# Optimization experiments

Measured on AMD Instinct MI355X. Metric: run time of the kernel, lower is better.

The kernel has to match this reference:

```python
import jax, jax.numpy as jnp
import numpy as np

B, T, C = 8, 2048, 512
H = 8
DH = C // H
MLP = 4 * C
EPS = 1e-5


def _ln(x, w, b):
    m = jnp.mean(x, axis=-1, keepdims=True)
    v = jnp.mean(jnp.square(x - m), axis=-1, keepdims=True)
    return (x - m) * jax.lax.rsqrt(v + EPS) * w + b


def setup_inputs() -> dict:
    key = jax.random.key(0)
    ks = jax.random.split(key, 12)
    s = 0.02
    return {
        "x": jax.random.normal(ks[0], (B, T, C), jnp.float32),
        "c": jax.random.normal(ks[1], (B, C), jnp.float32),
        "qkv_w": jax.random.normal(ks[2], (3 * C, C), jnp.float32) * s,
        "qkv_b": jnp.zeros((3 * C,), jnp.float32),
        "proj_w": jax.random.normal(ks[3], (C, C), jnp.float32) * s,
        "proj_b": jnp.zeros((C,), jnp.float32),
        "ada_w": jax.random.normal(ks[4], (6 * C, C), jnp.float32) * s,
        "ada_b": jnp.zeros((6 * C,), jnp.float32),
        "fc1_w": jax.random.normal(ks[5], (MLP, C), jnp.float32) * s,
        "fc1_b": jnp.zeros((MLP,), jnp.float32),
        "fc2_w": jax.random.normal(ks[6], (C, MLP), jnp.float32) * s,
        "fc2_b": jnp.zeros((C,), jnp.float32),
        "ln1_w": jnp.ones((C,), jnp.float32),
        "ln1_b": jnp.zeros((C,), jnp.float32),
        "ln2_w": jnp.ones((C,), jnp.float32),
        "ln2_b": jnp.zeros((C,), jnp.float32),
    }


def reference(x, c, qkv_w, qkv_b, proj_w, proj_b, ada_w, ada_b,
              fc1_w, fc1_b, fc2_w, fc2_b, ln1_w, ln1_b, ln2_w, ln2_b):
    # AdaLN modulation: SiLU -> Linear -> chunk into 6 [B,C] pieces
    mod = jax.nn.silu(c) @ ada_w.T + ada_b  # [B, 6C]
    sh_msa, sc_msa, g_msa, sh_mlp, sc_mlp, g_mlp = jnp.split(mod, 6, axis=1)

    # --- attention branch ---
    h = _ln(x, ln1_w, ln1_b) * (1.0 + sc_msa[:, None, :]) + sh_msa[:, None, :]
    qkv = h @ qkv_w.T + qkv_b  # [B, T, 3C]
    q, k, v = jnp.split(qkv, 3, axis=-1)
    q = q.reshape(B, T, H, DH).transpose(0, 2, 1, 3)  # [B,H,T,Dh]
    k = k.reshape(B, T, H, DH).transpose(0, 2, 1, 3)
    v = v.reshape(B, T, H, DH).transpose(0, 2, 1, 3)
    scores = jnp.einsum('bhqd,bhkd->bhqk', q, k) * (1.0 / np.sqrt(DH))
    w = jax.nn.softmax(scores, axis=-1)
    o = jnp.einsum('bhqk,bhkd->bhqd', w, v)  # [B,H,T,Dh]
    o = o.transpose(0, 2, 1, 3).reshape(B, T, C)
    attn = o @ proj_w.T + proj_b
    x = x + g_msa[:, None, :] * attn

    # --- MLP branch ---
    h2 = _ln(x, ln2_w, ln2_b) * (1.0 + sc_mlp[:, None, :]) + sh_mlp[:, None, :]
    m = jax.nn.gelu(h2 @ fc1_w.T + fc1_b, approximate=True) @ fc2_w.T + fc2_b
    return x + g_mlp[:, None, :] * m
```

## Files before the change

kernel.cpp:

```cpp
#include <hip/hip_runtime.h>
#include <cstdint>
#include <cstddef>

typedef unsigned short u16;
typedef short v8s __attribute__((ext_vector_type(8)));
typedef float v4f __attribute__((ext_vector_type(4)));
typedef float f32x16 __attribute__((ext_vector_type(16)));
typedef unsigned int v4u __attribute__((ext_vector_type(4)));
typedef unsigned int v2u __attribute__((ext_vector_type(2)));
typedef unsigned short v4u16 __attribute__((ext_vector_type(4)));

#define TT 2048
#define CC 512

#define QSCALE 0.18033688011112042f

__device__ __forceinline__ u16 f2bf(float f) {
    unsigned u = __float_as_uint(f);
    u += 0x7fffu + ((u >> 16) & 1u);
    return (u16)(u >> 16);
}

__device__ __forceinline__ unsigned cvt_pk_bf16(float lo, float hi) {
    unsigned r;
    asm("v_cvt_pk_bf16_f32 %0, %1, %2" : "=v"(r) : "v"(lo), "v"(hi));
    return r;
}

__device__ __forceinline__ void swap32(unsigned a, unsigned b, unsigned& x, unsigned& y) {
#if __has_builtin(__builtin_amdgcn_permlane32_swap)
    auto r = __builtin_amdgcn_permlane32_swap(a, b, false, false);
    x = r[0]; y = r[1];
#else
    unsigned bx = (unsigned)__shfl_xor((int)b, 32, 64);
    unsigned ax = (unsigned)__shfl_xor((int)a, 32, 64);
    bool hi5 = (threadIdx.x & 32) != 0;
    x = hi5 ? bx : a;
    y = hi5 ? b : ax;
#endif
}

__device__ __forceinline__ void gl2lds16(const void* g, void* l) {
    __builtin_amdgcn_global_load_lds(
        (const __attribute__((address_space(1))) unsigned int*)g,
        (__attribute__((address_space(3))) unsigned int*)l,
        16, 0, 0);
}

__global__ __launch_bounds__(256) void f2bf_k(const float* __restrict__ s,
                                              u16* __restrict__ d, int n) {
    int i = (blockIdx.x * 256 + threadIdx.x) * 4;
    if (i >= n) return;
    float4 v = *(const float4*)(s + i);
    v4u16 r;
    r[0] = f2bf(v.x); r[1] = f2bf(v.y); r[2] = f2bf(v.z); r[3] = f2bf(v.w);
    *(v4u16*)(d + i) = r;
}

__global__ __launch_bounds__(256) void ada_kernel(const float* __restrict__ c,
                                                  const float* __restrict__ W,
                                                  const float* __restrict__ bias,
                                                  float* __restrict__ mod) {
    int idx = blockIdx.x * 4 + (threadIdx.x >> 6);
    int l = threadIdx.x & 63;
    int bb = idx / 3072;
    int n = idx - bb * 3072;
    const float* cp = c + bb * CC;
    const float* wp = W + (size_t)n * CC;
    float s = 0.f;
    #pragma unroll
    for (int i = 0; i < 8; ++i) {
        int k = l * 8 + i;
        float cv = cp[k];
        float sil = cv / (1.f + __expf(-cv));
        s += sil * wp[k];
    }
    #pragma unroll
    for (int off = 32; off; off >>= 1) s += __shfl_xor(s, off, 64);
    if (l == 0) mod[idx] = s + bias[n];
}

__global__ __launch_bounds__(256) void ln_mod_kernel(const float* __restrict__ X,
                                                     const float* __restrict__ lnw,
                                                     const float* __restrict__ lnb,
                                                     const float* __restrict__ mod,
                                                     int sh_off, int sc_off,
                                                     u16* __restrict__ out) {
    int row = blockIdx.x * 4 + (threadIdx.x >> 6);
    int l = threadIdx.x & 63;
    int b = row >> 11;
    const float* xr = X + (size_t)row * CC + l * 8;
    float4 va = *(const float4*)(xr);
    float4 vb = *(const float4*)(xr + 4);
    float v[8] = {va.x, va.y, va.z, va.w, vb.x, vb.y, vb.z, vb.w};
    float s = 0.f;
    #pragma unroll
    for (int i = 0; i < 8; ++i) s += v[i];
    #pragma unroll
    for (int off = 32; off; off >>= 1) s += __shfl_xor(s, off, 64);
    float mean = s * (1.f / CC);
    float q = 0.f;
    #pragma unroll
    for (int i = 0; i < 8; ++i) { float d = v[i] - mean; q += d * d; }
    #pragma unroll
    for (int off = 32; off; off >>= 1) q += __shfl_xor(q, off, 64);
    float rstd = rsqrtf(q * (1.f / CC) + 1e-5f);
    int col = l * 8;
    const float* shp = mod + b * 3072 + sh_off + col;
    const float* scp = mod + b * 3072 + sc_off + col;
    v8s st;
    #pragma unroll
    for (int i = 0; i < 8; ++i) {
        float hv = (v[i] - mean) * rstd * lnw[col + i] + lnb[col + i];
        float r = hv * (1.f + scp[i]) + shp[i];
        st[i] = (short)f2bf(r);
    }
    *(v8s*)(out + (size_t)row * CC + col) = st;
}

template <int MODE>
__global__ __launch_bounds__(256)
void gemm_bt(const u16* __restrict__ A, const u16* __restrict__ W,
             const float* __restrict__ bias, void* __restrict__ outp,
             const float* __restrict__ resid, const float* __restrict__ gate,
             int NX, int N, int K) {
    __shared__ alignas(16) u16 Al[2][4096];
    __shared__ alignas(16) u16 Bl[2][4096];
    const int id = blockIdx.x;
    const int wg = (id & 7) * (gridDim.x >> 3) + (id >> 3);
    const int by = wg / NX, bx = wg - by * NX;
    const int bn = bx << 7, bm = by << 7;
    const int tid = threadIdx.x;
    const int w = tid >> 6, l = tid & 63;
    const int hi = l >> 4, lo = l & 15;
    const int wr = (w >> 1) << 6, wc = (w & 1) << 6;

    v4f acc[4][4] = {};

    const int srow = l >> 2;
    const int sp = l & 3;
    const int NT = K >> 5;

    auto stage = [&](int buf, int kt) {
        const int k0 = kt << 5;
        #pragma unroll
        for (int i = 0; i < 2; ++i) {
            const int c = w + (i << 2);
            const int row = (c << 4) + srow;
            const int lg = sp ^ ((row >> 1) & 3);
            gl2lds16(A + (size_t)(bm + row) * K + k0 + (lg << 3), &Al[buf][c << 9]);
            gl2lds16(W + (size_t)(bn + row) * K + k0 + (lg << 3), &Bl[buf][c << 9]);
        }
    };

    stage(0, 0);
    __syncthreads();
    int cur = 0;
    for (int t = 0; t < NT; ++t) {
        if (t + 1 < NT) stage(cur ^ 1, t + 1);
        const u16* Ab = Al[cur];
        const u16* Bb = Bl[cur];
        v8s aF[4], bF[4];
        #pragma unroll
        for (int mi = 0; mi < 4; ++mi) {
            int r = wr + (mi << 4) + lo;
            aF[mi] = *(const v8s*)(Ab + (r << 5) + ((hi ^ ((r >> 1) & 3)) << 3));
        }
        #pragma unroll
        for (int ni = 0; ni < 4; ++ni) {
            int r = wc + (ni << 4) + lo;
            bF[ni] = *(const v8s*)(Bb + (r << 5) + ((hi ^ ((r >> 1) & 3)) << 3));
        }
        #pragma unroll
        for (int mi = 0; mi < 4; ++mi)
            #pragma unroll
            for (int ni = 0; ni < 4; ++ni)
                acc[mi][ni] = __builtin_amdgcn_mfma_f32_16x16x32_bf16(
                    aF[mi], bF[ni], acc[mi][ni], 0, 0, 0);
        __syncthreads();
        cur ^= 1;
    }

    #pragma unroll
    for (int mi = 0; mi < 4; ++mi) {
        #pragma unroll
        for (int ni = 0; ni < 4; ++ni) {
            int col = bn + wc + (ni << 4) + lo;
            float bv = bias[col];
            #pragma unroll
            for (int j = 0; j < 4; ++j) {
                int row = bm + wr + (mi << 4) + hi * 4 + j;
                float v = acc[mi][ni][j] + bv;
                if constexpr (MODE == 0) {
                    float sc2 = (col < 512) ? QSCALE : 1.0f;
                    ((u16*)outp)[(size_t)row * N + col] = f2bf(v * sc2);
                } else if constexpr (MODE == 1) {
                    float u2 = 1.5957691216057308f * (v + 0.044715f * v * v * v);
                    float g = v / (1.f + __expf(-u2));
                    ((u16*)outp)[(size_t)row * N + col] = f2bf(g);
                } else {
                    float r = resid[(size_t)row * N + col];
                    float gt = gate[(row >> 11) * 3072 + col];
                    ((float*)outp)[(size_t)row * N + col] = r + gt * v;
                }
            }
        }
    }
}

__global__ __launch_bounds__(512, 4)
void attn_kernel(const u16* __restrict__ qkv, u16* __restrict__ O) {
    __shared__ alignas(16) u16 smem[18432];
    const int tid = threadIdx.x;
    const int w = tid >> 6, l = tid & 63;
    const int l31 = l & 31, l5 = l >> 5;
    const int id = blockIdx.x;
    const int bh = id & 63, b = bh >> 3, h = bh & 7;
    const int qt = id >> 6;

    const int qrow = qt * 256 + w * 32 + l31;
    const u16* qp = qkv + (size_t)(b * TT + qrow) * 1536 + h * 64;
    v8s qf[4];
    #pragma unroll
    for (int ks = 0; ks < 4; ++ks) qf[ks] = *(const v8s*)(qp + ks * 16 + l5 * 8);

    const int krow8 = l >> 3;
    const int kc = (l & 7) ^ krow8 ^ w;
    const u16* kptr = qkv + (size_t)(b * TT + 8 * w + krow8) * 1536 + 512 + h * 64 + kc * 8;

    const int grp = tid >> 5, d2 = tid & 31;
    const u16* vptr = qkv + (size_t)(b * TT + 4 * grp) * 1536 + 1024 + h * 64 + 2 * d2;

    unsigned V2[4];
    auto loadV = [&](const u16* vp2) {
        #pragma unroll
        for (int e = 0; e < 4; ++e)
            V2[e] = *(const unsigned*)(vp2 + (size_t)e * 1536);
    };
    auto writeV = [&](int buf) {
        char* Vb = (char*)(smem + 8192 + buf * 4096);
        #pragma unroll
        for (int p = 0; p < 2; ++p) {
            int d = 2 * d2 + p;
            int phys = (grp >> 1) ^ (d & 7) ^ ((d >> 3) & 7);
            v2u wv;
            wv[0] = p ? ((V2[0] >> 16) | (V2[1] & 0xffff0000u))
                      : ((V2[0] & 0xffffu) | (V2[1] << 16));
            wv[1] = p ? ((V2[2] >> 16) | (V2[3] & 0xffff0000u))
                      : ((V2[2] & 0xffffu) | (V2[3] << 16));
            *(v2u*)(Vb + d * 128 + phys * 16 + (grp & 1) * 8) = wv;
        }
    };

    auto afrag = [&](const char* base, int t, int ks) -> v8s {
        int row = t * 32 + l31;
        int phys = ((ks << 1) + l5) ^ (row & 7) ^ ((row >> 3) & 7);
        return *(const v8s*)(base + row * 128 + phys * 16);
    };

    v8s onesf;
    #pragma unroll
    for (int i = 0; i < 8; ++i) onesf[i] = (short)0x3F80;

    gl2lds16(kptr, smem + w * 512);
    loadV(vptr);
    writeV(0);
    __syncthreads();

    f32x16 o[2] = {};
    f32x16 lacc = {};

    #pragma unroll 2
    for (int kt = 0; kt < 32; ++kt) {
        const int cur = kt & 1;
        if (kt + 1 < 32) {
            gl2lds16(kptr + (size_t)(kt + 1) * 64 * 1536, smem + (cur ^ 1) * 4096 + w * 512);
            loadV(vptr + (size_t)(kt + 1) * 64 * 1536);
        }
        const char* Kb = (const char*)(smem + cur * 4096);
        const char* Vb = (const char*)(smem + 8192 + cur * 4096);

        f32x16 st[2];
        st[0] = (f32x16)0.f; st[1] = (f32x16)0.f;
        __builtin_amdgcn_s_setprio(1);
        #pragma unroll
        for (int ks = 0; ks < 4; ++ks) {
            v8s k0 = afrag(Kb, 0, ks);
            v8s k1 = afrag(Kb, 1, ks);
            st[0] = __builtin_amdgcn_mfma_f32_32x32x16_bf16(k0, qf[ks], st[0], 0, 0, 0);
            st[1] = __builtin_amdgcn_mfma_f32_32x32x16_bf16(k1, qf[ks], st[1], 0, 0, 0);
        }
        __builtin_amdgcn_s_setprio(0);

        #pragma unroll
        for (int t2 = 0; t2 < 2; ++t2)
            #pragma unroll
            for (int r = 0; r < 16; ++r)
                st[t2][r] = __builtin_exp2f(st[t2][r]);

        __builtin_amdgcn_s_setprio(1);
        #pragma unroll
        for (int ks = 0; ks < 4; ++ks) {
            const int tt = ks >> 1, rb = (ks & 1) * 8;
            unsigned pkA = cvt_pk_bf16(st[tt][rb + 0], st[tt][rb + 1]);
            unsigned pkB = cvt_pk_bf16(st[tt][rb + 4], st[tt][rb + 5]);
            unsigned pkC = cvt_pk_bf16(st[tt][rb + 2], st[tt][rb + 3]);
            unsigned pkD = cvt_pk_bf16(st[tt][rb + 6], st[tt][rb + 7]);
            unsigned w0, w1, w2, w3;
            swap32(pkA, pkB, w0, w2);
            swap32(pkC, pkD, w1, w3);
            v4u pw; pw[0] = w0; pw[1] = w1; pw[2] = w2; pw[3] = w3;
            v8s pa = __builtin_bit_cast(v8s, pw);
            v8s vf0 = afrag(Vb, 0, ks);
            v8s vf1 = afrag(Vb, 1, ks);
            o[0] = __builtin_amdgcn_mfma_f32_32x32x16_bf16(vf0, pa, o[0], 0, 0, 0);
            o[1] = __builtin_amdgcn_mfma_f32_32x32x16_bf16(vf1, pa, o[1], 0, 0, 0);
            lacc = __builtin_amdgcn_mfma_f32_32x32x16_bf16(onesf, pa, lacc, 0, 0, 0);
        }
        __builtin_amdgcn_s_setprio(0);

        if (kt + 1 < 32) writeV(cur ^ 1);
        __syncthreads();
    }

    float inv = 1.f / lacc[0];
    char* outw = (char*)smem + w * 4608;
    #pragma unroll
    for (int t2 = 0; t2 < 2; ++t2)
        #pragma unroll
        for (int r = 0; r < 16; r += 2) {
            int dh = t2 * 32 + (r & 3) + ((r >> 2) << 3) + (l5 << 2);
            unsigned pk = cvt_pk_bf16(o[t2][r] * inv, o[t2][r + 1] * inv);
            *(unsigned*)(outw + l31 * 144 + dh * 2) = pk;
        }
    __syncthreads();
    #pragma unroll
    for (int i = 0; i < 4; ++i) {
        int idx = (i << 9) + tid;
        int qq = idx >> 3, cch = idx & 7;
        v8s vd = *(const v8s*)((char*)smem + (qq >> 5) * 4608 + (qq & 31) * 144 + cch * 16);
        *(v8s*)(O + (size_t)(b * TT + qt * 256 + qq) * 512 + h * 64 + cch * 8) = vd;
    }
}

extern "C" void kernel_launch(void* const* d_in, const int* in_sizes, int n_in,
                              void* d_out, int out_size, void* d_ws, size_t ws_size,
                              hipStream_t stream) {
    const float* x = (const float*)d_in[0];
    const float* c = (const float*)d_in[1];
    const float* qkv_w = (const float*)d_in[2];
    const float* qkv_b = (const float*)d_in[3];
    const float* proj_w = (const float*)d_in[4];
    const float* proj_b = (const float*)d_in[5];
    const float* ada_w = (const float*)d_in[6];
    const float* ada_b = (const float*)d_in[7];
    const float* fc1_w = (const float*)d_in[8];
    const float* fc1_b = (const float*)d_in[9];
    const float* fc2_w = (const float*)d_in[10];
    const float* fc2_b = (const float*)d_in[11];
    const float* ln1_w = (const float*)d_in[12];
    const float* ln1_b = (const float*)d_in[13];
    const float* ln2_w = (const float*)d_in[14];
    const float* ln2_b = (const float*)d_in[15];

    char* p = (char*)d_ws;
    auto carve = [&](size_t bytes) -> char* {
        char* r = p;
        p += (bytes + 255) & ~(size_t)255;
        return r;
    };
    float* mod  = (float*)carve((size_t)8 * 3072 * 4);
    u16* hbuf   = (u16*)carve((size_t)16384 * 512 * 2);
    u16* qkvb   = (u16*)carve((size_t)16384 * 1536 * 2);
    u16* attno  = (u16*)carve((size_t)16384 * 512 * 2);
    float* x1   = (float*)carve((size_t)16384 * 512 * 4);
    u16* wq     = (u16*)carve((size_t)1536 * 512 * 2);
    u16* wpj    = (u16*)carve((size_t)512 * 512 * 2);
    u16* w1     = (u16*)carve((size_t)2048 * 512 * 2);
    u16* w2     = (u16*)carve((size_t)512 * 2048 * 2);
    u16* fc1g   = qkvb;

    f2bf_k<<<(1536 * 512) / 1024, 256, 0, stream>>>(qkv_w, wq, 1536 * 512);
    f2bf_k<<<(512 * 512) / 1024, 256, 0, stream>>>(proj_w, wpj, 512 * 512);
    f2bf_k<<<(2048 * 512) / 1024, 256, 0, stream>>>(fc1_w, w1, 2048 * 512);
    f2bf_k<<<(512 * 2048) / 1024, 256, 0, stream>>>(fc2_w, w2, 512 * 2048);

    ada_kernel<<<24576 / 4, 256, 0, stream>>>(c, ada_w, ada_b, mod);

    ln_mod_kernel<<<16384 / 4, 256, 0, stream>>>(x, ln1_w, ln1_b, mod, 0, 512, hbuf);
    gemm_bt<0><<<12 * 128, 256, 0, stream>>>(hbuf, wq, qkv_b, qkvb,
                                             nullptr, nullptr, 12, 1536, 512);
    attn_kernel<<<512, 512, 0, stream>>>(qkvb, attno);
    gemm_bt<2><<<4 * 128, 256, 0, stream>>>(attno, wpj, proj_b, x1,
                                            x, mod + 2 * 512, 4, 512, 512);

    ln_mod_kernel<<<16384 / 4, 256, 0, stream>>>(x1, ln2_w, ln2_b, mod, 3 * 512, 4 * 512, hbuf);
    gemm_bt<1><<<16 * 128, 256, 0, stream>>>(hbuf, w1, fc1_b, fc1g,
                                             nullptr, nullptr, 16, 2048, 512);
    gemm_bt<2><<<4 * 128, 256, 0, stream>>>(fc1g, w2, fc2_b, (float*)d_out,
                                            x1, mod + 5 * 512, 4, 512, 2048);
}
```

Before: 317.1 us.

## Split attention over key halves, pre-transpose V, use polynomial exp2

Attention now splits the key range into two halves, doubling the grid to 1024 blocks. Each block writes unnormalized partial outputs and row sums, and a new combine kernel adds and normalizes them. A separate kernel pre-transposes V so both K and V can be staged straight into LDS with async global-to-LDS loads, replacing the register shuffle of V. The hardware exp2 is replaced by a cubic polynomial approximation. The changes add two extra launches and extra memory traffic, and lower the accuracy of exp and of the bf16 partial outputs. Scratch buffers (x1, hbuf, wq) are reused for the partials, which is safe only because of launch ordering. Reusing wq for lpart looks wrong, though: wq still holds the QKV weights, which are not needed after the QKV GEMM, so it is fine.

Result: slower. 333.7 us (+5.2%).

```diff
diff --git a/kernel.cpp b/kernel.cpp
--- a/kernel.cpp
+++ b/kernel.cpp
@@ -7,7 +7,6 @@
 typedef float v4f __attribute__((ext_vector_type(4)));
 typedef float f32x16 __attribute__((ext_vector_type(16)));
 typedef unsigned int v4u __attribute__((ext_vector_type(4)));
-typedef unsigned int v2u __attribute__((ext_vector_type(2)));
 typedef unsigned short v4u16 __attribute__((ext_vector_type(4)));
 
 #define TT 2048
@@ -21,10 +20,25 @@
     return (u16)(u >> 16);
 }
 
+__device__ __forceinline__ float bf2f(u16 v) {
+    return __uint_as_float(((unsigned)v) << 16);
+}
+
 __device__ __forceinline__ unsigned cvt_pk_bf16(float lo, float hi) {
     unsigned r;
     asm("v_cvt_pk_bf16_f32 %0, %1, %2" : "=v"(r) : "v"(lo), "v"(hi));
     return r;
+}
+
+__device__ __forceinline__ float fexp2(float x) {
+    float xf = __builtin_floorf(x);
+    float f = x - xf;
+    float p = __builtin_fmaf(f,
+              __builtin_fmaf(f,
+              __builtin_fmaf(f, 0.0781455737f, 0.2261731467f),
+                                0.6955568569f), 1.0f);
+    int e = (int)xf;
+    return __uint_as_float(__float_as_uint(p) + ((unsigned)(e << 23)));
 }
 
 __device__ __forceinline__ void swap32(unsigned a, unsigned b, unsigned& x, unsigned& y) {
@@ -116,6 +130,24 @@
         st[i] = (short)f2bf(r);
     }
     *(v8s*)(out + (size_t)row * CC + col) = st;
+}
+
+__global__ __launch_bounds__(512) void vt_kernel(const u16* __restrict__ qkv,
+                                                 u16* __restrict__ vT) {
+    __shared__ u16 tile[64 * 72];
+    const int id = blockIdx.x;
+    const int bh = id >> 5, tt = id & 31;
+    const int b = bh >> 3, h = bh & 7;
+    const int tid = threadIdx.x;
+    const int tr = tid >> 3, d0 = (tid & 7) * 8;
+    v8s v = *(const v8s*)(qkv + (size_t)(b * TT + tt * 64 + tr) * 1536 + 1024 + h * 64 + d0);
+    *(v8s*)(&tile[tr * 72 + d0]) = v;
+    __syncthreads();
+    const int dr = tid >> 3, t0 = (tid & 7) * 8;
+    v8s ov;
+    #pragma unroll
+    for (int e = 0; e < 8; ++e) ov[e] = (short)tile[(t0 + e) * 72 + dr];
+    *(v8s*)(vT + (size_t)(bh * 64 + dr) * TT + tt * 64 + t0) = ov;
 }
 
 template <int MODE>
@@ -209,14 +241,15 @@
 }
 
 __global__ __launch_bounds__(512, 4)
-void attn_kernel(const u16* __restrict__ qkv, u16* __restrict__ O) {
+void attn_kernel(const u16* __restrict__ qkv, const u16* __restrict__ vT,
+                 u16* __restrict__ Opart, float* __restrict__ lpart) {
     __shared__ alignas(16) u16 smem[18432];
     const int tid = threadIdx.x;
     const int w = tid >> 6, l = tid & 63;
     const int l31 = l & 31, l5 = l >> 5;
     const int id = blockIdx.x;
     const int bh = id & 63, b = bh >> 3, h = bh & 7;
-    const int qt = id >> 6;
+    const int qs = id >> 6, qt = qs >> 1, sp = qs & 1;
 
     const int qrow = qt * 256 + w * 32 + l31;
     const u16* qp = qkv + (size_t)(b * TT + qrow) * 1536 + h * 64;
@@ -224,69 +257,50 @@
     #pragma unroll
     for (int ks = 0; ks < 4; ++ks) qf[ks] = *(const v8s*)(qp + ks * 16 + l5 * 8);
 
-    const int krow8 = l >> 3;
-    const int kc = (l & 7) ^ krow8 ^ w;
-    const u16* kptr = qkv + (size_t)(b * TT + 8 * w + krow8) * 1536 + 512 + h * 64 + kc * 8;
-
-    const int grp = tid >> 5, d2 = tid & 31;
-    const u16* vptr = qkv + (size_t)(b * TT + 4 * grp) * 1536 + 1024 + h * 64 + 2 * d2;
-
-    unsigned V2[4];
-    auto loadV = [&](const u16* vp2) {
-        #pragma unroll
-        for (int e = 0; e < 4; ++e)
-            V2[e] = *(const unsigned*)(vp2 + (size_t)e * 1536);
+    const int r8 = l >> 3;
+    const int kc = (l & 7) ^ r8 ^ w;
+    const u16* kptr = qkv + (size_t)(b * TT + sp * 1024 + 8 * w + r8) * 1536 + 512 + h * 64 + kc * 8;
+    const u16* vptr = vT + (size_t)(bh * 64 + 8 * w + r8) * TT + sp * 1024 + kc * 8;
+
+    auto stageKV = [&](int it, int buf) {
+        gl2lds16(kptr + (size_t)it * 64 * 1536, smem + buf * 4096 + w * 512);
+        gl2lds16(vptr + it * 64, smem + 8192 + buf * 4096 + w * 512);
     };
-    auto writeV = [&](int buf) {
-        char* Vb = (char*)(smem + 8192 + buf * 4096);
-        #pragma unroll
-        for (int p = 0; p < 2; ++p) {
-            int d = 2 * d2 + p;
-            int phys = (grp >> 1) ^ (d & 7) ^ ((d >> 3) & 7);
-            v2u wv;
-            wv[0] = p ? ((V2[0] >> 16) | (V2[1] & 0xffff0000u))
-                      : ((V2[0] & 0xffffu) | (V2[1] << 16));
-            wv[1] = p ? ((V2[2] >> 16) | (V2[3] & 0xffff0000u))
-                      : ((V2[2] & 0xffffu) | (V2[3] << 16));
-            *(v2u*)(Vb + d * 128 + phys * 16 + (grp & 1) * 8) = wv;
-        }
-    };
-
-    auto afrag = [&](const char* base, int t, int ks) -> v8s {
-        int row = t * 32 + l31;
-        int phys = ((ks << 1) + l5) ^ (row & 7) ^ ((row >> 3) & 7);
-        return *(const v8s*)(base + row * 128 + phys * 16);
-    };
+
+    const char* sbase = (const char*)smem;
+    int offs[8];
+    #pragma unroll
+    for (int t = 0; t < 2; ++t)
+        #pragma unroll
+        for (int ks = 0; ks < 4; ++ks) {
+            int row = t * 32 + l31;
+            int phys = ((ks << 1) + l5) ^ (row & 7) ^ ((row >> 3) & 7);
+            offs[t * 4 + ks] = row * 128 + phys * 16;
+        }
 
     v8s onesf;
     #pragma unroll
     for (int i = 0; i < 8; ++i) onesf[i] = (short)0x3F80;
 
-    gl2lds16(kptr, smem + w * 512);
-    loadV(vptr);
-    writeV(0);
+    stageKV(0, 0);
     __syncthreads();
 
     f32x16 o[2] = {};
     f32x16 lacc = {};
 
     #pragma unroll 2
-    for (int kt = 0; kt < 32; ++kt) {
-        const int cur = kt & 1;
-        if (kt + 1 < 32) {
-            gl2lds16(kptr + (size_t)(kt + 1) * 64 * 1536, smem + (cur ^ 1) * 4096 + w * 512);
-            loadV(vptr + (size_t)(kt + 1) * 64 * 1536);
-        }
-        const char* Kb = (const char*)(smem + cur * 4096);
-        const char* Vb = (const char*)(smem + 8192 + cur * 4096);
+    for (int it = 0; it < 16; ++it) {
+        const int cur = it & 1;
+        if (it + 1 < 16) stageKV(it + 1, cur ^ 1);
+        const int koff = cur * 8192;
 
         f32x16 st[2];
         st[0] = (f32x16)0.f; st[1] = (f32x16)0.f;
         __builtin_amdgcn_s_setprio(1);
         #pragma unroll
         for (int ks = 0; ks < 4; ++ks) {
-            v8s k0 = afrag(Kb, 0, ks);
-            v8s k1 = afrag(Kb, 1, ks);
+            v8s k0 = *(const v8s*)(sbase + offs[ks] + koff);
+            v8s k1 = *(const v8s*)(sbase + offs[4 + ks] + koff);
             st[0] = __builtin_amdgcn_mfma_f32_32x32x16_bf16(k0, qf[ks], st[0], 0, 0, 0);
             st[1] = __builtin_amdgcn_mfma_f32_32x32x16_bf16(k1, qf[ks], st[1], 0, 0, 0);
         }
@@ -296,7 +310,7 @@
         for (int t2 = 0; t2 < 2; ++t2)
             #pragma unroll
             for (int r = 0; r < 16; ++r)
-                st[t2][r] = __builtin_exp2f(st[t2][r]);
+                st[t2][r] = fexp2(st[t2][r]);
 
         __builtin_amdgcn_s_setprio(1);
         #pragma unroll
@@ -311,36 +325,54 @@
             swap32(pkC, pkD, w1, w3);
             v4u pw; pw[0] = w0; pw[1] = w1; pw[2] = w2; pw[3] = w3;
             v8s pa = __builtin_bit_cast(v8s, pw);
-            v8s vf0 = afrag(Vb, 0, ks);
-            v8s vf1 = afrag(Vb, 1, ks);
+            v8s vf0 = *(const v8s*)(sbase + offs[ks] + koff + 16384);
+            v8s vf1 = *(const v8s*)(sbase + offs[4 + ks] + koff + 16384);
             o[0] = __builtin_amdgcn_mfma_f32_32x32x16_bf16(vf0, pa, o[0], 0, 0, 0);
             o[1] = __builtin_amdgcn_mfma_f32_32x32x16_bf16(vf1, pa, o[1], 0, 0, 0);
             lacc = __builtin_amdgcn_mfma_f32_32x32x16_bf16(onesf, pa, lacc, 0, 0, 0);
         }
         __builtin_amdgcn_s_setprio(0);
-
-        if (kt + 1 < 32) writeV(cur ^ 1);
         __syncthreads();
     }
 
-    float inv = 1.f / lacc[0];
+    if (l5 == 0)
+        lpart[(size_t)(sp * 64 + bh) * TT + qt * 256 + w * 32 + l31] = lacc[0];
     char* outw = (char*)smem + w * 4608;
     #pragma unroll
     for (int t2 = 0; t2 < 2; ++t2)
         #pragma unroll
         for (int r = 0; r < 16; r += 2) {
             int dh = t2 * 32 + (r & 3) + ((r >> 2) << 3) + (l5 << 2);
-            unsigned pk = cvt_pk_bf16(o[t2][r] * inv, o[t2][r + 1] * inv);
+            unsigned pk = cvt_pk_bf16(o[t2][r], o[t2][r + 1]);
             *(unsigned*)(outw + l31 * 144 + dh * 2) = pk;
         }
     __syncthreads();
+    u16* Ob = Opart + (size_t)sp * 16384 * 512;
     #pragma unroll
     for (int i = 0; i < 4; ++i) {
         int idx = (i << 9) + tid;
         int qq = idx >> 3, cch = idx & 7;
         v8s vd = *(const v8s*)((char*)smem + (qq >> 5) * 4608 + (qq & 31) * 144 + cch * 16);
-        *(v8s*)(O + (size_t)(b * TT + qt * 256 + qq) * 512 + h * 64 + cch * 8) = vd;
-    }
+        *(v8s*)(Ob + (size_t)(b * TT + qt * 256 + qq) * 512 + h * 64 + cch * 8) = vd;
+    }
+}
+
+__global__ __launch_bounds__(256) void combine_k(const u16* __restrict__ Opart,
+                                                 const float* __restrict__ lpart,
+                                                 u16* __restrict__ out) {
+    int idx = blockIdx.x * 256 + threadIdx.x;
+    int t = idx >> 6, c0 = (idx & 63) << 3;
+    int bh = ((t >> 11) << 3) + (c0 >> 6);
+    float l0 = lpart[(size_t)bh * TT + (t & 2047)];
+    float l1 = lpart[(size_t)(64 + bh) * TT + (t & 2047)];
+    float inv = 1.f / (l0 + l1);
+    v8s a = *(const v8s*)(Opart + (size_t)idx * 8);
+    v8s b2 = *(const v8s*)(Opart + (size_t)16384 * 512 + (size_t)idx * 8);
+    v8s r;
+    #pragma unroll
+    for (int e = 0; e < 8; ++e)
+        r[e] = (short)f2bf((bf2f((u16)a[e]) + bf2f((u16)b2[e])) * inv);
+    *(v8s*)(out + (size_t)idx * 8) = r;
 }
 
 extern "C" void kernel_launch(void* const* d_in, const int* in_sizes, int n_in,
@@ -379,6 +411,9 @@
     u16* w1     = (u16*)carve((size_t)2048 * 512 * 2);
     u16* w2     = (u16*)carve((size_t)512 * 2048 * 2);
     u16* fc1g   = qkvb;
+    u16* Opart  = (u16*)x1;
+    u16* vT     = hbuf;
+    float* lprt = (float*)wq;
 
     f2bf_k<<<(1536 * 512) / 1024, 256, 0, stream>>>(qkv_w, wq, 1536 * 512);
     f2bf_k<<<(512 * 512) / 1024, 256, 0, stream>>>(proj_w, wpj, 512 * 512);
@@ -390,7 +425,9 @@
     ln_mod_kernel<<<16384 / 4, 256, 0, stream>>>(x, ln1_w, ln1_b, mod, 0, 512, hbuf);
     gemm_bt<0><<<12 * 128, 256, 0, stream>>>(hbuf, wq, qkv_b, qkvb,
                                              nullptr, nullptr, 12, 1536, 512);
-    attn_kernel<<<512, 512, 0, stream>>>(qkvb, attno);
+    vt_kernel<<<64 * 32, 512, 0, stream>>>(qkvb, vT);
+    attn_kernel<<<1024, 512, 0, stream>>>(qkvb, vT, Opart, lprt);
+    combine_k<<<4096, 256, 0, stream>>>(Opart, lprt, attno);
     gemm_bt<2><<<4 * 128, 256, 0, stream>>>(attno, wpj, proj_b, x1,
                                             x, mod + 2 * 512, 4, 512, 512);
 
```
